# Kernel optimization log

Hardware: AMD Instinct MI355X
Metric: run time of the kernel (lower is better)

Reference implementation:

```python
import jax, jax.numpy as jnp
import numpy as np

N, CIN, H, W_ = 16, 64, 56, 56
COUT, K, STRIDE, PAD = 64, 3, 1, 1


def setup_inputs() -> dict:
    key = jax.random.key(0)
    k1, k2 = jax.random.split(key)
    x = jax.random.normal(k1, (N, CIN, H, W_), dtype=jnp.float32)
    adder = jax.random.normal(k2, (COUT, CIN, K, K), dtype=jnp.float32)
    return {"x": x, "adder": adder}


def reference(x, adder):
    # AdderNet 2d: out[n,co,h,w] = -sum_{ci,kh,kw} |patch(n,:,h,w) - adder[co]|
    n, c, h, w = x.shape
    co = adder.shape[0]
    # im2col: [N, C*K*K, Ho, Wo]; feature dim ordered (c, kh, kw), matching
    # torch.nn.functional.unfold and adder.reshape(Co, C*K*K).
    patches = jax.lax.conv_general_dilated_patches(
        x, filter_shape=(K, K), window_strides=(STRIDE, STRIDE),
        padding=((PAD, PAD), (PAD, PAD)))
    n_, ckk, ho, wo = patches.shape
    p = patches.reshape(n_, ckk, ho * wo)          # [N, CKK, L]
    w_col = adder.reshape(co, ckk)                 # [Co, CKK]

    def per_filter(wf):
        # wf: [CKK]; negative L1 distance of this filter to every patch
        return -jnp.sum(jnp.abs(p - wf[None, :, None]), axis=1)  # [N, L]

    # Sequential map over output channels avoids materializing the full
    # [Co, N, CKK, L] broadcast tensor (~7 GB); peak extra memory is one
    # [N, CKK, L] diff buffer per step.
    out = jax.lax.map(per_filter, w_col)           # [Co, N, L]
    out = out.transpose(1, 0, 2).reshape(n_, co, ho, wo)
    return out
```

## Files before the change

### kernel.cpp

```cpp
#include <hip/hip_runtime.h>

#define N_    16
#define CIN_  64
#define HW_   56
#define COUT_ 64
#define HP    58
#define HPSQ  (HP * HP)

typedef float f4u __attribute__((ext_vector_type(4), aligned(4)));

__global__ void pad_x_kernel(const float* __restrict__ x, float* __restrict__ xp) {
    int idx = blockIdx.x * 256 + threadIdx.x;
    const int total = N_ * CIN_ * HPSQ;
    if (idx >= total) return;
    int w  = idx % HP;
    int t  = idx / HP;
    int h  = t % HP;
    int nc = t / HP;
    float v = 0.f;
    if (h >= 1 && h <= HW_ && w >= 1 && w <= HW_)
        v = x[((size_t)nc * HW_ + (h - 1)) * HW_ + (w - 1)];
    xp[idx] = v;
}

__global__ __launch_bounds__(256, 4) void adder_main_kernel(
    const float* __restrict__ xp, const float* __restrict__ wt,
    float* __restrict__ out) {
    __shared__ float red[3][64][49];

    int bid  = blockIdx.x;
    int n    = bid >> 6;
    int co   = bid & 63;
    int tid  = threadIdx.x;
    int wid  = tid >> 6;
    int lane = tid & 63;
    int tx   = lane & 7;
    int ty   = lane >> 3;
    int h0   = ty * 7;
    int w0   = tx * 7;

    const float* xbase = xp + (size_t)n * CIN_ * HPSQ + h0 * HP + w0;
    const float* wbase = wt + (size_t)co * 576;

    float acc[7][7] = {};

    const int ci0 = wid * 16;
    for (int ci = ci0; ci < ci0 + 16; ++ci) {
        const float* xc  = xbase + (size_t)ci * HPSQ;
        const float* wci = wbase + ci * 9;
        float w[9];
        #pragma unroll
        for (int k = 0; k < 9; ++k) w[k] = wci[k];

        float buf[9][9];
        #define LOADROW(r) { \
            f4u a_ = *(const f4u*)(xc + (r) * HP);      \
            f4u b_ = *(const f4u*)(xc + (r) * HP + 4);  \
            buf[r][0] = a_.x; buf[r][1] = a_.y; buf[r][2] = a_.z; buf[r][3] = a_.w; \
            buf[r][4] = b_.x; buf[r][5] = b_.y; buf[r][6] = b_.z; buf[r][7] = b_.w; \
            buf[r][8] = xc[(r) * HP + 8]; }
        #define COMP(oh) { \
            _Pragma("unroll") \
            for (int kh = 0; kh < 3; ++kh) { \
                _Pragma("unroll") \
                for (int kw = 0; kw < 3; ++kw) { \
                    float wv = w[kh * 3 + kw]; \
                    _Pragma("unroll") \
                    for (int j = 0; j < 7; ++j) \
                        acc[oh][j] += fabsf(buf[(oh) + kh][j + kw] - wv); \
                } } }

        LOADROW(0) LOADROW(1) LOADROW(2)
        COMP(0)
        LOADROW(3) COMP(1)
        LOADROW(4) COMP(2)
        LOADROW(5) COMP(3)
        LOADROW(6) COMP(4)
        LOADROW(7) COMP(5)
        LOADROW(8) COMP(6)
        #undef LOADROW
        #undef COMP
    }

    if (wid != 0) {
        float* rp = &red[wid - 1][lane][0];
        #pragma unroll
        for (int oh = 0; oh < 7; ++oh)
            #pragma unroll
            for (int j = 0; j < 7; ++j) rp[oh * 7 + j] = acc[oh][j];
    }
    __syncthreads();
    if (wid == 0) {
        float* ob = out + (((size_t)(n * COUT_ + co)) * HW_ + h0) * HW_ + w0;
        #pragma unroll
        for (int oh = 0; oh < 7; ++oh)
            #pragma unroll
            for (int j = 0; j < 7; ++j) {
                float s = acc[oh][j]
                        + red[0][lane][oh * 7 + j]
                        + red[1][lane][oh * 7 + j]
                        + red[2][lane][oh * 7 + j];
                ob[oh * HW_ + j] = -s;
            }
    }
}

extern "C" void kernel_launch(void* const* d_in, const int* in_sizes, int n_in,
                              void* d_out, int out_size, void* d_ws, size_t ws_size,
                              hipStream_t stream) {
    const float* x     = (const float*)d_in[0];
    const float* adder = (const float*)d_in[1];
    float* out = (float*)d_out;

    float* xp = (float*)d_ws;

    const int padTotal = N_ * CIN_ * HPSQ;
    pad_x_kernel<<<(padTotal + 255) / 256, 256, 0, stream>>>(x, xp);
    adder_main_kernel<<<N_ * COUT_, 256, 0, stream>>>(xp, adder, out);
}
```

Baseline: 187.8 us.

## Stage input planes into LDS with double-buffered async loads, two output channels per block

Measured after the change: 200.1 us. 6.5% more time.

```diff
diff --git a/kernel.cpp b/kernel.cpp
--- a/kernel.cpp
+++ b/kernel.cpp
@@ -4,105 +4,120 @@
 #define CIN_  64
 #define HW_   56
 #define COUT_ 64
-#define HP    58
-#define HPSQ  (HP * HP)
-
-typedef float f4u __attribute__((ext_vector_type(4), aligned(4)));
+#define HPR   58
+#define WST   60
+#define PLANE (HPR * WST)
+#define PLANE_PAD 3584
 
 __global__ void pad_x_kernel(const float* __restrict__ x, float* __restrict__ xp) {
     int idx = blockIdx.x * 256 + threadIdx.x;
-    const int total = N_ * CIN_ * HPSQ;
+    const int total = N_ * CIN_ * PLANE_PAD;
     if (idx >= total) return;
-    int w  = idx % HP;
-    int t  = idx / HP;
-    int h  = t % HP;
-    int nc = t / HP;
+    int rem = idx % PLANE_PAD;
+    int nc  = idx / PLANE_PAD;
+    int h   = rem / WST;
+    int w   = rem % WST;
     float v = 0.f;
     if (h >= 1 && h <= HW_ && w >= 1 && w <= HW_)
         v = x[((size_t)nc * HW_ + (h - 1)) * HW_ + (w - 1)];
     xp[idx] = v;
 }
 
-__global__ __launch_bounds__(256, 4) void adder_main_kernel(
+__global__ __launch_bounds__(256, 2) void adder_main_kernel(
     const float* __restrict__ xp, const float* __restrict__ wt,
     float* __restrict__ out) {
-    __shared__ float red[3][64][49];
+    __shared__ float lds[2][2][PLANE_PAD];
 
-    int bid  = blockIdx.x;
-    int n    = bid >> 6;
-    int co   = bid & 63;
-    int tid  = threadIdx.x;
-    int wid  = tid >> 6;
-    int lane = tid & 63;
-    int tx   = lane & 7;
-    int ty   = lane >> 3;
-    int h0   = ty * 7;
-    int w0   = tx * 7;
+    const int bid  = blockIdx.x;
+    const int n    = bid >> 5;
+    const int cop  = bid & 31;
+    const int tid  = threadIdx.x;
+    const int wid  = tid >> 6;
+    const int lane = tid & 63;
+    const int coidx  = wid >> 1;
+    const int cihalf = wid & 1;
+    const int co   = cop * 2 + coidx;
+    const int tx = lane & 7, ty = lane >> 3;
+    const int h0 = ty * 7, w0 = tx * 7;
 
-    const float* xbase = xp + (size_t)n * CIN_ * HPSQ + h0 * HP + w0;
-    const float* wbase = wt + (size_t)co * 576;
+    const int sgH = wid >> 1;
+    const int sgW = wid & 1;
+    const size_t gplane0 = (size_t)(n * CIN_) * PLANE_PAD;
+
+    #define STAGEP(bufi, ci_) { \
+        const float* gsrc_ = xp + gplane0 + (size_t)(sgH * 32 + (ci_)) * PLANE_PAD; \
+        float* ldst_ = &lds[bufi][sgH][0]; \
+        _Pragma("unroll") \
+        for (int k_ = 0; k_ < 7; ++k_) { \
+            int ch_ = k_ * 2 + sgW; \
+            __builtin_amdgcn_global_load_lds( \
+                (const __attribute__((address_space(1))) void*)(gsrc_ + ch_ * 256 + lane * 4), \
+                (__attribute__((address_space(3))) void*)(ldst_ + ch_ * 256), 16, 0, 0); \
+        } }
 
     float acc[7][7] = {};
+    const int rb = h0 * WST + w0;
 
-    const int ci0 = wid * 16;
-    for (int ci = ci0; ci < ci0 + 16; ++ci) {
-        const float* xc  = xbase + (size_t)ci * HPSQ;
-        const float* wci = wbase + ci * 9;
-        float w[9];
+    STAGEP(0, 0)
+    __syncthreads();
+
+    for (int it = 0; it < 32; ++it) {
+        const int cur = it & 1;
+        if (it < 31) STAGEP(cur ^ 1, it + 1)
+
+        const float* lp = &lds[cur][cihalf][0];
+        const int ci = cihalf * 32 + it;
+        const float* wp = wt + (size_t)co * 576 + (size_t)ci * 9;
+        float w9[9];
         #pragma unroll
-        for (int k = 0; k < 9; ++k) w[k] = wci[k];
+        for (int k = 0; k < 9; ++k) w9[k] = wp[k];
 
         float buf[9][9];
-        #define LOADROW(r) { \
-            f4u a_ = *(const f4u*)(xc + (r) * HP);      \
-            f4u b_ = *(const f4u*)(xc + (r) * HP + 4);  \
-            buf[r][0] = a_.x; buf[r][1] = a_.y; buf[r][2] = a_.z; buf[r][3] = a_.w; \
-            buf[r][4] = b_.x; buf[r][5] = b_.y; buf[r][6] = b_.z; buf[r][7] = b_.w; \
-            buf[r][8] = xc[(r) * HP + 8]; }
-        #define COMP(oh) { \
-            _Pragma("unroll") \
+        #define LROW(r) { _Pragma("unroll") \
+            for (int c = 0; c < 9; ++c) buf[r][c] = lp[rb + (r) * WST + c]; }
+        #define CROW(oh) { _Pragma("unroll") \
             for (int kh = 0; kh < 3; ++kh) { \
                 _Pragma("unroll") \
                 for (int kw = 0; kw < 3; ++kw) { \
-                    float wv = w[kh * 3 + kw]; \
+                    float wv = w9[kh * 3 + kw]; \
                     _Pragma("unroll") \
                     for (int j = 0; j < 7; ++j) \
                         acc[oh][j] += fabsf(buf[(oh) + kh][j + kw] - wv); \
                 } } }
 
-        LOADROW(0) LOADROW(1) LOADROW(2)
-        COMP(0)
-        LOADROW(3) COMP(1)
-        LOADROW(4) COMP(2)
-        LOADROW(5) COMP(3)
-        LOADROW(6) COMP(4)
-        LOADROW(7) COMP(5)
-        LOADROW(8) COMP(6)
-        #undef LOADROW
-        #undef COMP
+        LROW(0) LROW(1) LROW(2) LROW(3)
+        CROW(0) LROW(4)
+        CROW(1) LROW(5)
+        CROW(2) LROW(6)
+        CROW(3) LROW(7)
+        CROW(4) LROW(8)
+        CROW(5)
+        CROW(6)
+        #undef LROW
+        #undef CROW
+
+        __syncthreads();
     }
 
-    if (wid != 0) {
-        float* rp = &red[wid - 1][lane][0];
+    float* red = &lds[0][0][0];
+    if (cihalf == 1) {
+        float* rp = red + (size_t)(coidx * 64 + lane) * 49;
         #pragma unroll
         for (int oh = 0; oh < 7; ++oh)
             #pragma unroll
             for (int j = 0; j < 7; ++j) rp[oh * 7 + j] = acc[oh][j];
     }
     __syncthreads();
-    if (wid == 0) {
+    if (cihalf == 0) {
+        const float* rp = red + (size_t)(coidx * 64 + lane) * 49;
         float* ob = out + (((size_t)(n * COUT_ + co)) * HW_ + h0) * HW_ + w0;
         #pragma unroll
         for (int oh = 0; oh < 7; ++oh)
             #pragma unroll
-            for (int j = 0; j < 7; ++j) {
-                float s = acc[oh][j]
-                        + red[0][lane][oh * 7 + j]
-                        + red[1][lane][oh * 7 + j]
-                        + red[2][lane][oh * 7 + j];
-                ob[oh * HW_ + j] = -s;
-            }
+            for (int j = 0; j < 7; ++j)
+                ob[oh * HW_ + j] = -(acc[oh][j] + rp[oh * 7 + j]);
     }
+    #undef STAGEP
 }
 
 extern "C" void kernel_launch(void* const* d_in, const int* in_sizes, int n_in,
@@ -114,7 +129,7 @@
 
     float* xp = (float*)d_ws;
 
-    const int padTotal = N_ * CIN_ * HPSQ;
+    const int padTotal = N_ * CIN_ * PLANE_PAD;
     pad_x_kernel<<<(padTotal + 255) / 256, 256, 0, stream>>>(x, xp);
-    adder_main_kernel<<<N_ * COUT_, 256, 0, stream>>>(xp, adder, out);
+    adder_main_kernel<<<N_ * 32, 256, 0, stream>>>(xp, adder, out);
 }
```
